# Kernel optimization log

Hardware: AMD Instinct MI355X
Metric: run time of the kernel (lower is better)

The kernel has to match this reference:

```python
import jax, jax.numpy as jnp
import numpy as np

N_STYLE_TOKEN = 10
TOKEN_SIZE = 256   # num_units
NUM_HEADS = 8
D_K = TOKEN_SIZE // NUM_HEADS  # 32, key_dim of cross-attention
D_Q = 256                      # encoder_hidden (add_gst=True, add_positional_encoding=True)
MAX_SEQ_LEN = 2000


def sinusoid_table(n_pos, d):
    pos = np.arange(n_pos, dtype=np.float64)[:, None]
    i = np.arange(d, dtype=np.float64)[None, :]
    angle = pos / np.power(10000.0, 2.0 * (i // 2) / d)
    table = np.zeros((n_pos, d), dtype=np.float64)
    table[:, 0::2] = np.sin(angle[:, 0::2])
    table[:, 1::2] = np.cos(angle[:, 1::2])
    return jnp.asarray(table, dtype=jnp.float32)


def setup_inputs() -> dict:
    key = jax.random.key(0)
    k1, k2, k3, k4, k5, k6 = jax.random.split(key, 6)
    N, T = 64, 2000
    inputs = jax.random.normal(k1, (N, T, D_Q), dtype=jnp.float32)
    positional_indexes = jnp.sort(
        jax.random.randint(k2, (N, T), 0, T), axis=-1).astype(jnp.int64)
    embed = 0.5 * jax.random.normal(k3, (N_STYLE_TOKEN, D_K), dtype=jnp.float32)
    # nn.Linear(in, out, bias=False) weights stored as [out, in]
    Wq = jax.random.normal(k4, (TOKEN_SIZE, D_Q), dtype=jnp.float32) / np.sqrt(D_Q)
    Wk = jax.random.normal(k5, (TOKEN_SIZE, D_K), dtype=jnp.float32) / np.sqrt(D_K)
    Wv = jax.random.normal(k6, (TOKEN_SIZE, D_K), dtype=jnp.float32) / np.sqrt(D_K)
    pos_table = sinusoid_table(MAX_SEQ_LEN + 1, D_Q)  # non-trainable buffer
    return {"inputs": inputs, "positional_indexes": positional_indexes,
            "embed": embed, "Wq": Wq, "Wk": Wk, "Wv": Wv,
            "pos_table": pos_table}


def reference(inputs, positional_indexes, embed, Wq, Wk, Wv, pos_table):
    N, T, dq = inputs.shape
    H, ds = NUM_HEADS, TOKEN_SIZE // NUM_HEADS
    n_tok, d_k = embed.shape

    # per-utterance positional gather (the python for-loop, vectorized):
    # pos_enc_by_scale[i, t] = pos_table[positional_indexes[i, t]]
    pos_enc = pos_table[positional_indexes]            # [N, T, dq]
    x = inputs + pos_enc                               # add_positional_encoding=True

    keys = jnp.tanh(embed)                             # [n_tok, d_k]

    q = jnp.einsum('ntq,uq->ntu', x, Wq)               # [N, T, U]
    k = keys @ Wk.T                                    # [n_tok, U]
    v = keys @ Wv.T                                    # [n_tok, U]

    qh = q.reshape(N, T, H, ds)                        # split heads along units
    kh = k.reshape(n_tok, H, ds)
    vh = v.reshape(n_tok, H, ds)

    logits = jnp.einsum('nthd,khd->nhtk', qh, kh) / jnp.sqrt(
        jnp.asarray(d_k, dtype=qh.dtype))              # [N, H, T, n_tok]
    attn = jax.nn.softmax(logits, axis=-1)

    out = jnp.einsum('nhtk,khd->nthd', attn, vh).reshape(N, T, H * ds)
    # scores: [h,N,T,k] pieces concatenated on last dim, then transpose(1,2)
    scores = jnp.transpose(attn, (0, 1, 3, 2)).reshape(N, H * n_tok, T)
    return out, scores
```

## Files before the change

### kernel.cpp

```cpp
#include <hip/hip_runtime.h>

#define T_SEQ 2000
#define N_UTT 64
#define DQ 256
#define NTOK 10
#define NH 8
#define DS 32
#define NC 80
#define LGS 84

typedef float f32x4 __attribute__((ext_vector_type(4)));
typedef short s16x8 __attribute__((ext_vector_type(8)));

__device__ __forceinline__ unsigned short f2bf(float f){
    unsigned int u = __float_as_uint(f);
    u += 0x7FFFu + ((u >> 16) & 1u);
    return (unsigned short)(u >> 16);
}
__device__ __forceinline__ float bf2f(unsigned short h){
    return __uint_as_float(((unsigned int)h) << 16);
}

__global__ __launch_bounds__(256) void prep_kv(
    const float* __restrict__ embed, const float* __restrict__ Wk,
    const float* __restrict__ Wv, float* __restrict__ khd, float* __restrict__ vhd)
{
    __shared__ float th[NTOK*DS];
    const int u = threadIdx.x;
    for (int i = u; i < NTOK*DS; i += 256) th[i] = tanhf(embed[i]);
    __syncthreads();
    for (int tok = 0; tok < NTOK; ++tok){
        float ka = 0.f, va = 0.f;
        #pragma unroll
        for (int d = 0; d < DS; ++d){
            const float kd = th[tok*DS + d];
            ka += kd * Wk[u*DS + d];
            va += kd * Wv[u*DS + d];
        }
        khd[tok*DQ + u] = ka;
        vhd[tok*DQ + u] = va;
    }
}

__global__ __launch_bounds__(256) void prep_wl(
    const float* __restrict__ Wq, const float* __restrict__ khd,
    unsigned short* __restrict__ WlH, unsigned short* __restrict__ WlL)
{
    const int c = blockIdx.x;
    const int q = threadIdx.x;
    const int h = c / NTOK, tok = c - h*NTOK;
    float s = 0.f;
    #pragma unroll
    for (int d = 0; d < DS; ++d)
        s += Wq[(size_t)(h*DS + d)*DQ + q] * khd[tok*DQ + h*DS + d];
    s *= 0.17677669529663687f;
    const unsigned short hi = f2bf(s);
    const unsigned short lo = f2bf(s - bf2f(hi));
    WlH[c*DQ + q] = hi;
    WlL[c*DQ + q] = lo;
}

__global__ __launch_bounds__(64, 4) void main_kernel(
    const float* __restrict__ inputs, const int* __restrict__ pidx,
    const float* __restrict__ pos_table, const unsigned short* __restrict__ WlH,
    const unsigned short* __restrict__ WlL, const float* __restrict__ vhd,
    float* __restrict__ outp, float* __restrict__ scores)
{
    __shared__ float lg[2][16][LGS];
    const int lane = threadIdx.x;
    const int lrow = lane & 15;
    const int quad = lane >> 4;
    const int m0   = blockIdx.x * 32;

    const int rowA = m0 + lrow;
    const int rowB = rowA + 16;
    const int idxA = pidx[rowA];
    const int idxB = pidx[rowB];

    f32x4 acc[2][5] = {};

    for (int kt = 0; kt < 8; ++kt){
        const int kq = kt*32 + quad*8;
        s16x8 ah[2], al[2];
        #pragma unroll
        for (int mt = 0; mt < 2; ++mt){
            const float* xp = inputs    + (size_t)(mt ? rowB : rowA)*DQ + kq;
            const float* pp = pos_table + (size_t)(mt ? idxB : idxA)*DQ + kq;
            f32x4 x0 = *(const f32x4*)xp;
            f32x4 x1 = *(const f32x4*)(xp + 4);
            x0 += *(const f32x4*)pp;
            x1 += *(const f32x4*)(pp + 4);
            s16x8 h8, l8;
            #pragma unroll
            for (int j = 0; j < 4; ++j){
                const unsigned short hv = f2bf(x0[j]);
                h8[j]   = (short)hv;
                l8[j]   = (short)f2bf(x0[j] - bf2f(hv));
                const unsigned short hw = f2bf(x1[j]);
                h8[4+j] = (short)hw;
                l8[4+j] = (short)f2bf(x1[j] - bf2f(hw));
            }
            ah[mt] = h8; al[mt] = l8;
        }
        #pragma unroll
        for (int ct = 0; ct < 5; ++ct){
            const s16x8 bh = *(const s16x8*)(WlH + (ct*16 + lrow)*DQ + kq);
            const s16x8 bl = *(const s16x8*)(WlL + (ct*16 + lrow)*DQ + kq);
            #pragma unroll
            for (int mt = 0; mt < 2; ++mt){
                acc[mt][ct] = __builtin_amdgcn_mfma_f32_16x16x32_bf16(al[mt], bh, acc[mt][ct], 0,0,0);
                acc[mt][ct] = __builtin_amdgcn_mfma_f32_16x16x32_bf16(ah[mt], bl, acc[mt][ct], 0,0,0);
                acc[mt][ct] = __builtin_amdgcn_mfma_f32_16x16x32_bf16(ah[mt], bh, acc[mt][ct], 0,0,0);
            }
        }
    }

    #pragma unroll
    for (int mt = 0; mt < 2; ++mt)
        #pragma unroll
        for (int ct = 0; ct < 5; ++ct)
            #pragma unroll
            for (int reg = 0; reg < 4; ++reg)
                lg[mt][quad*4 + reg][ct*16 + lrow] = acc[mt][ct][reg];

    const int r = lrow;
    #pragma unroll
    for (int hh = 0; hh < 2; ++hh){
        const int h = quad + hh*4;
        float p[2][NTOK];
        #pragma unroll
        for (int mt = 0; mt < 2; ++mt){
            float lv[NTOK];
            #pragma unroll
            for (int k = 0; k < NTOK; ++k) lv[k] = lg[mt][r][h*NTOK + k];
            float mx = lv[0];
            #pragma unroll
            for (int k = 1; k < NTOK; ++k) mx = fmaxf(mx, lv[k]);
            float s = 0.f;
            #pragma unroll
            for (int k = 0; k < NTOK; ++k){ p[mt][k] = __expf(lv[k] - mx); s += p[mt][k]; }
            const float inv = 1.f / s;
            const int row = m0 + mt*16 + r;
            const int n = row / T_SEQ;
            const int t = row - n*T_SEQ;
            float* sp = scores + (size_t)(n*(NH*NTOK) + h*NTOK)*T_SEQ + t;
            #pragma unroll
            for (int k = 0; k < NTOK; ++k){
                p[mt][k] *= inv;
                sp[(size_t)k*T_SEQ] = p[mt][k];
            }
        }
        float* o0 = outp + (size_t)(m0 + r)*DQ + h*DS;
        float* o1 = outp + (size_t)(m0 + 16 + r)*DQ + h*DS;
        #pragma unroll
        for (int db = 0; db < 8; ++db){
            f32x4 a0 = {}, a1 = {};
            #pragma unroll
            for (int k = 0; k < NTOK; ++k){
                const f32x4 vv = *(const f32x4*)(vhd + k*DQ + h*DS + db*4);
                a0 += p[0][k] * vv;
                a1 += p[1][k] * vv;
            }
            *(f32x4*)(o0 + db*4) = a0;
            *(f32x4*)(o1 + db*4) = a1;
        }
    }
}

extern "C" void kernel_launch(void* const* d_in, const int* in_sizes, int n_in,
                              void* d_out, int out_size, void* d_ws, size_t ws_size,
                              hipStream_t stream)
{
    const float* inputs    = (const float*)d_in[0];
    const int*   pidx      = (const int*)d_in[1];
    const float* embed     = (const float*)d_in[2];
    const float* Wq        = (const float*)d_in[3];
    const float* Wk        = (const float*)d_in[4];
    const float* Wv        = (const float*)d_in[5];
    const float* pos_table = (const float*)d_in[6];

    float* outp   = (float*)d_out;
    float* scores = outp + (size_t)N_UTT*T_SEQ*DQ;

    float* khd = (float*)d_ws;
    float* vhd = khd + NTOK*DQ;
    unsigned short* WlH = (unsigned short*)(vhd + NTOK*DQ);
    unsigned short* WlL = WlH + NC*DQ;

    prep_kv<<<1, 256, 0, stream>>>(embed, Wk, Wv, khd, vhd);
    prep_wl<<<NC, 256, 0, stream>>>(Wq, khd, WlH, WlL);
    main_kernel<<<(N_UTT*T_SEQ)/32, 64, 0, stream>>>(inputs, pidx, pos_table,
                                                     WlH, WlL, vhd, outp, scores);
}
```

Baseline: 392.8 us.

## Drop weight low-part split and retile main kernel to one 16-row tile per wave

Measured after the change: 435.0 us. 10.7% more time.

```diff
diff --git a/kernel.cpp b/kernel.cpp
--- a/kernel.cpp
+++ b/kernel.cpp
@@ -44,7 +44,7 @@
 
 __global__ __launch_bounds__(256) void prep_wl(
     const float* __restrict__ Wq, const float* __restrict__ khd,
-    unsigned short* __restrict__ WlH, unsigned short* __restrict__ WlL)
+    unsigned short* __restrict__ WlH)
 {
     const int c = blockIdx.x;
     const int q = threadIdx.x;
@@ -54,115 +54,92 @@
     for (int d = 0; d < DS; ++d)
         s += Wq[(size_t)(h*DS + d)*DQ + q] * khd[tok*DQ + h*DS + d];
     s *= 0.17677669529663687f;
-    const unsigned short hi = f2bf(s);
-    const unsigned short lo = f2bf(s - bf2f(hi));
-    WlH[c*DQ + q] = hi;
-    WlL[c*DQ + q] = lo;
+    WlH[c*DQ + q] = f2bf(s);
 }
 
-__global__ __launch_bounds__(64, 4) void main_kernel(
+__global__ __launch_bounds__(128, 8) void main_kernel(
     const float* __restrict__ inputs, const int* __restrict__ pidx,
     const float* __restrict__ pos_table, const unsigned short* __restrict__ WlH,
-    const unsigned short* __restrict__ WlL, const float* __restrict__ vhd,
+    const float* __restrict__ vhd,
     float* __restrict__ outp, float* __restrict__ scores)
 {
     __shared__ float lg[2][16][LGS];
-    const int lane = threadIdx.x;
+    const int wave = threadIdx.x >> 6;
+    const int lane = threadIdx.x & 63;
     const int lrow = lane & 15;
     const int quad = lane >> 4;
-    const int m0   = blockIdx.x * 32;
+    const int m0   = (blockIdx.x * 2 + wave) * 16;
 
-    const int rowA = m0 + lrow;
-    const int rowB = rowA + 16;
-    const int idxA = pidx[rowA];
-    const int idxB = pidx[rowB];
+    const int row = m0 + lrow;
+    const int idx = pidx[row];
+    const float* xr = inputs    + (size_t)row*DQ;
+    const float* pr = pos_table + (size_t)idx*DQ;
 
-    f32x4 acc[2][5] = {};
+    f32x4 acc[5] = {};
 
+    #pragma unroll
     for (int kt = 0; kt < 8; ++kt){
         const int kq = kt*32 + quad*8;
-        s16x8 ah[2], al[2];
+        f32x4 x0 = *(const f32x4*)(xr + kq);
+        f32x4 x1 = *(const f32x4*)(xr + kq + 4);
+        x0 += *(const f32x4*)(pr + kq);
+        x1 += *(const f32x4*)(pr + kq + 4);
+        s16x8 h8, l8;
         #pragma unroll
-        for (int mt = 0; mt < 2; ++mt){
-            const float* xp = inputs    + (size_t)(mt ? rowB : rowA)*DQ + kq;
-            const float* pp = pos_table + (size_t)(mt ? idxB : idxA)*DQ + kq;
-            f32x4 x0 = *(const f32x4*)xp;
-            f32x4 x1 = *(const f32x4*)(xp + 4);
-            x0 += *(const f32x4*)pp;
-            x1 += *(const f32x4*)(pp + 4);
-            s16x8 h8, l8;
-            #pragma unroll
-            for (int j = 0; j < 4; ++j){
-                const unsigned short hv = f2bf(x0[j]);
-                h8[j]   = (short)hv;
-                l8[j]   = (short)f2bf(x0[j] - bf2f(hv));
-                const unsigned short hw = f2bf(x1[j]);
-                h8[4+j] = (short)hw;
-                l8[4+j] = (short)f2bf(x1[j] - bf2f(hw));
-            }
-            ah[mt] = h8; al[mt] = l8;
+        for (int j = 0; j < 4; ++j){
+            const unsigned short hv = f2bf(x0[j]);
+            h8[j]   = (short)hv;
+            l8[j]   = (short)f2bf(x0[j] - bf2f(hv));
+            const unsigned short hw = f2bf(x1[j]);
+            h8[4+j] = (short)hw;
+            l8[4+j] = (short)f2bf(x1[j] - bf2f(hw));
         }
         #pragma unroll
         for (int ct = 0; ct < 5; ++ct){
             const s16x8 bh = *(const s16x8*)(WlH + (ct*16 + lrow)*DQ + kq);
-            const s16x8 bl = *(const s16x8*)(WlL + (ct*16 + lrow)*DQ + kq);
-            #pragma unroll
-            for (int mt = 0; mt < 2; ++mt){
-                acc[mt][ct] = __builtin_amdgcn_mfma_f32_16x16x32_bf16(al[mt], bh, acc[mt][ct], 0,0,0);
-                acc[mt][ct] = __builtin_amdgcn_mfma_f32_16x16x32_bf16(ah[mt], bl, acc[mt][ct], 0,0,0);
-                acc[mt][ct] = __builtin_amdgcn_mfma_f32_16x16x32_bf16(ah[mt], bh, acc[mt][ct], 0,0,0);
-            }
+            acc[ct] = __builtin_amdgcn_mfma_f32_16x16x32_bf16(l8, bh, acc[ct], 0,0,0);
+            acc[ct] = __builtin_amdgcn_mfma_f32_16x16x32_bf16(h8, bh, acc[ct], 0,0,0);
         }
     }
 
     #pragma unroll
-    for (int mt = 0; mt < 2; ++mt)
+    for (int ct = 0; ct < 5; ++ct)
         #pragma unroll
-        for (int ct = 0; ct < 5; ++ct)
-            #pragma unroll
-            for (int reg = 0; reg < 4; ++reg)
-                lg[mt][quad*4 + reg][ct*16 + lrow] = acc[mt][ct][reg];
+        for (int reg = 0; reg < 4; ++reg)
+            lg[wave][quad*4 + reg][ct*16 + lrow] = acc[ct][reg];
 
-    const int r = lrow;
+    const int n  = m0 / T_SEQ;
+    const int t  = (m0 - n*T_SEQ) + lrow;
+    const int r  = lrow;
     #pragma unroll
     for (int hh = 0; hh < 2; ++hh){
         const int h = quad + hh*4;
-        float p[2][NTOK];
+        float lv[NTOK];
         #pragma unroll
-        for (int mt = 0; mt < 2; ++mt){
-            float lv[NTOK];
-            #pragma unroll
-            for (int k = 0; k < NTOK; ++k) lv[k] = lg[mt][r][h*NTOK + k];
-            float mx = lv[0];
-            #pragma unroll
-            for (int k = 1; k < NTOK; ++k) mx = fmaxf(mx, lv[k]);
-            float s = 0.f;
-            #pragma unroll
-            for (int k = 0; k < NTOK; ++k){ p[mt][k] = __expf(lv[k] - mx); s += p[mt][k]; }
-            const float inv = 1.f / s;
-            const int row = m0 + mt*16 + r;
-            const int n = row / T_SEQ;
-            const int t = row - n*T_SEQ;
-            float* sp = scores + (size_t)(n*(NH*NTOK) + h*NTOK)*T_SEQ + t;
-            #pragma unroll
-            for (int k = 0; k < NTOK; ++k){
-                p[mt][k] *= inv;
-                sp[(size_t)k*T_SEQ] = p[mt][k];
-            }
+        for (int k = 0; k < NTOK; ++k) lv[k] = lg[wave][r][h*NTOK + k];
+        float mx = lv[0];
+        #pragma unroll
+        for (int k = 1; k < NTOK; ++k) mx = fmaxf(mx, lv[k]);
+        float p[NTOK], s = 0.f;
+        #pragma unroll
+        for (int k = 0; k < NTOK; ++k){ p[k] = __expf(lv[k] - mx); s += p[k]; }
+        const float inv = 1.f / s;
+        float* sp = scores + (size_t)(n*(NH*NTOK) + h*NTOK)*T_SEQ + t;
+        #pragma unroll
+        for (int k = 0; k < NTOK; ++k){
+            p[k] *= inv;
+            sp[(size_t)k*T_SEQ] = p[k];
         }
-        float* o0 = outp + (size_t)(m0 + r)*DQ + h*DS;
-        float* o1 = outp + (size_t)(m0 + 16 + r)*DQ + h*DS;
+        float* o = outp + (size_t)row*DQ + h*DS;
         #pragma unroll
         for (int db = 0; db < 8; ++db){
-            f32x4 a0 = {}, a1 = {};
+            f32x4 a = {};
             #pragma unroll
             for (int k = 0; k < NTOK; ++k){
                 const f32x4 vv = *(const f32x4*)(vhd + k*DQ + h*DS + db*4);
-                a0 += p[0][k] * vv;
-                a1 += p[1][k] * vv;
+                a += p[k] * vv;
             }
-            *(f32x4*)(o0 + db*4) = a0;
-            *(f32x4*)(o1 + db*4) = a1;
+            *(f32x4*)(o + db*4) = a;
         }
     }
 }
@@ -185,10 +162,9 @@
     float* khd = (float*)d_ws;
     float* vhd = khd + NTOK*DQ;
     unsigned short* WlH = (unsigned short*)(vhd + NTOK*DQ);
-    unsigned short* WlL = WlH + NC*DQ;
 
     prep_kv<<<1, 256, 0, stream>>>(embed, Wk, Wv, khd, vhd);
-    prep_wl<<<NC, 256, 0, stream>>>(Wq, khd, WlH, WlL);
-    main_kernel<<<(N_UTT*T_SEQ)/32, 64, 0, stream>>>(inputs, pidx, pos_table,
-                                                     WlH, WlL, vhd, outp, scores);
+    prep_wl<<<NC, 256, 0, stream>>>(Wq, khd, WlH);
+    main_kernel<<<(N_UTT*T_SEQ)/32, 128, 0, stream>>>(inputs, pidx, pos_table,
+                                                      WlH, vhd, outp, scores);
 }
```
